# Optimization experiments

Hardware: AMD Instinct MI355X
Metric: run time of the kernel (lower is better)

Reference implementation:

```python
import jax, jax.numpy as jnp
import numpy as np

NORM_EPS = 1e-12  # torch F.normalize default eps (module's self.eps is unused)


def setup_inputs() -> dict:
    key = jax.random.key(0)
    k1, k2 = jax.random.split(key)
    src_feat = jax.random.normal(k1, (4, 2048, 128), dtype=jnp.float32)
    tgt_feat = jax.random.normal(k2, (4, 2048, 128), dtype=jnp.float32)
    return {"src_feat": src_feat, "tgt_feat": tgt_feat}


def reference(src_feat, tgt_feat):
    # src_feat: [B,N,C], tgt_feat: [B,M,C]
    # Cosine similarity via normalized matmul instead of [B,N,M,C] broadcast.
    src_sq = jnp.sum(src_feat * src_feat, axis=-1)          # [B,N]
    tgt_sq = jnp.sum(tgt_feat * tgt_feat, axis=-1)          # [B,M]
    src_n = src_feat / jnp.maximum(jnp.sqrt(src_sq), NORM_EPS)[..., None]
    tgt_n = tgt_feat / jnp.maximum(jnp.sqrt(tgt_sq), NORM_EPS)[..., None]
    cosine_sim = jnp.einsum('bnc,bmc->bnm', src_n, tgt_n)   # [B,N,M]
    # Squared L2 distance via ||s||^2 + ||t||^2 - 2 s.t (clamped for numerics)
    dots = jnp.einsum('bnc,bmc->bnm', src_feat, tgt_feat)   # [B,N,M]
    dist_sq = src_sq[:, :, None] + tgt_sq[:, None, :] - 2.0 * dots
    feat_dist = jnp.sqrt(jnp.maximum(dist_sq, 0.0))
    feat_dist_normalized = 1.0 / (1.0 + feat_dist)
    # [B,N,M,2]
    return jnp.stack([cosine_sim, feat_dist_normalized], axis=-1)
```

## Files before the change

### kernel.cpp

```cpp
#include <hip/hip_runtime.h>

#define BATCH 4
#define NDIM 2048
#define MDIM 2048
#define CDIM 128

typedef short bf16x8 __attribute__((ext_vector_type(8)));
typedef float f32x4  __attribute__((ext_vector_type(4)));

__device__ __forceinline__ unsigned short f2bf(float f) {
    union { float f; unsigned int u; } v; v.f = f;
    unsigned int u = v.u;
    return (unsigned short)((u + 0x7FFFu + ((u >> 16) & 1u)) >> 16);
}

__global__ __launch_bounds__(256) void norm_kernel(
    const float* __restrict__ src, const float* __restrict__ tgt,
    float* __restrict__ ws)
{
    int gid  = blockIdx.x * 256 + threadIdx.x;
    int wid  = gid >> 6;
    int lane = gid & 63;
    const float* base = (wid < BATCH * NDIM)
        ? (src + (size_t)wid * CDIM)
        : (tgt + (size_t)(wid - BATCH * NDIM) * CDIM);
    float2 v = ((const float2*)base)[lane];
    float s = v.x * v.x + v.y * v.y;
    #pragma unroll
    for (int off = 32; off >= 1; off >>= 1) s += __shfl_xor(s, off, 64);
    if (lane == 0) ws[wid] = s;
}

__global__ __launch_bounds__(256) void sim_mfma(
    const float* __restrict__ src, const float* __restrict__ tgt,
    const float* __restrict__ ws, float* __restrict__ out)
{
    __shared__ unsigned short As[128 * 128];
    __shared__ unsigned short Bs[128 * 128];

    const int tid = threadIdx.x;
    const int b   = blockIdx.z;
    const int i0  = blockIdx.y << 7;
    const int j0  = blockIdx.x << 7;

    const float4* s4 = (const float4*)(src + ((size_t)b * NDIM + i0) * CDIM);
    const float4* t4 = (const float4*)(tgt + ((size_t)b * MDIM + j0) * CDIM);

    #pragma unroll 4
    for (int it = 0; it < 16; ++it) {
        int idx  = tid + it * 256;
        int row  = idx >> 5;
        int c4   = idx & 31;
        float4 va = s4[idx];
        float4 vb = t4[idx];
        int chunk = c4 >> 1;
        int half  = c4 & 1;
        int off   = row * 128 + (((chunk ^ (row & 15)) << 3) + (half << 2));
        ushort4 ua, ub;
        ua.x = f2bf(va.x); ua.y = f2bf(va.y); ua.z = f2bf(va.z); ua.w = f2bf(va.w);
        ub.x = f2bf(vb.x); ub.y = f2bf(vb.y); ub.z = f2bf(vb.z); ub.w = f2bf(vb.w);
        *(ushort4*)&As[off] = ua;
        *(ushort4*)&Bs[off] = ub;
    }
    __syncthreads();

    const int wave = tid >> 6;
    const int lane = tid & 63;
    const int wm   = (wave & 1) << 6;
    const int wn   = (wave >> 1) << 6;
    const int l16  = lane & 15;
    const int q    = lane >> 4;

    f32x4 acc[4][4];
    #pragma unroll
    for (int i = 0; i < 4; ++i)
        #pragma unroll
        for (int j = 0; j < 4; ++j) acc[i][j] = (f32x4){0.f, 0.f, 0.f, 0.f};

    #pragma unroll
    for (int k0 = 0; k0 < 4; ++k0) {
        int chunk = (k0 << 2) + q;
        int swz   = (chunk ^ l16) << 3;
        bf16x8 a[4], bv[4];
        #pragma unroll
        for (int i = 0; i < 4; ++i)
            a[i] = *(const bf16x8*)&As[(wm + (i << 4) + l16) * 128 + swz];
        #pragma unroll
        for (int j = 0; j < 4; ++j)
            bv[j] = *(const bf16x8*)&Bs[(wn + (j << 4) + l16) * 128 + swz];
        #pragma unroll
        for (int i = 0; i < 4; ++i)
            #pragma unroll
            for (int j = 0; j < 4; ++j)
                acc[i][j] = __builtin_amdgcn_mfma_f32_16x16x32_bf16(
                    a[i], bv[j], acc[i][j], 0, 0, 0);
    }

    const float* nrmS = ws + (size_t)b * NDIM + i0;
    const float* nrmT = ws + (size_t)BATCH * NDIM + (size_t)b * MDIM + j0;

    float sq[4][4], isq[4][4];
    #pragma unroll
    for (int i = 0; i < 4; ++i) {
        float4 s4v = *(const float4*)&nrmS[wm + (i << 4) + (q << 2)];
        sq[i][0] = s4v.x; sq[i][1] = s4v.y; sq[i][2] = s4v.z; sq[i][3] = s4v.w;
        #pragma unroll
        for (int r = 0; r < 4; ++r)
            isq[i][r] = __builtin_amdgcn_rsqf(fmaxf(sq[i][r], 1e-24f));
    }
    float tq[4], itq[4];
    #pragma unroll
    for (int j = 0; j < 4; ++j) {
        tq[j]  = nrmT[wn + (j << 4) + l16];
        itq[j] = __builtin_amdgcn_rsqf(fmaxf(tq[j], 1e-24f));
    }

    float2* out2 = (float2*)out;
    #pragma unroll
    for (int i = 0; i < 4; ++i) {
        #pragma unroll
        for (int r = 0; r < 4; ++r) {
            int mrow = wm + (i << 4) + (q << 2) + r;
            size_t rowbase = ((size_t)b * NDIM + (size_t)(i0 + mrow)) * MDIM + j0;
            float sqr = sq[i][r], isr = isq[i][r];
            #pragma unroll
            for (int j = 0; j < 4; ++j) {
                int ncol = wn + (j << 4) + l16;
                float d   = acc[i][j][r];
                float cs  = d * isr * itq[j];
                float dsq = sqr + tq[j] - 2.0f * d;
                float fd  = __builtin_amdgcn_sqrtf(fmaxf(dsq, 0.0f));
                float fdn = __builtin_amdgcn_rcpf(1.0f + fd);
                out2[rowbase + ncol] = make_float2(cs, fdn);
            }
        }
    }
}

extern "C" void kernel_launch(void* const* d_in, const int* in_sizes, int n_in,
                              void* d_out, int out_size, void* d_ws, size_t ws_size,
                              hipStream_t stream) {
    const float* src = (const float*)d_in[0];
    const float* tgt = (const float*)d_in[1];
    float* ws  = (float*)d_ws;
    float* out = (float*)d_out;

    norm_kernel<<<dim3(4096), dim3(256), 0, stream>>>(src, tgt, ws);

    dim3 grid(MDIM / 128, NDIM / 128, BATCH);
    sim_mfma<<<grid, dim3(256), 0, stream>>>(src, tgt, ws, out);
}
```

Baseline: 147.8 us.

## Halve N tile, interleave MFMA with epilogue, widen norm kernel loads

The similarity kernel's tile shrinks from 128x128 to 128x64 and shared memory for B is halved. The launch bound now requests 3 blocks per SM, and the MFMA accumulation is split into two 16-column passes, each followed straight away by its epilogue. This cuts live accumulator registers and LDS use to raise occupancy and overlap output stores with compute, at the cost of twice as many blocks that each reload the A tile. The norm kernel now processes two rows per wave with float4 loads.

```diff
diff --git a/kernel.cpp b/kernel.cpp
--- a/kernel.cpp
+++ b/kernel.cpp
@@ -21,27 +21,28 @@
     int gid  = blockIdx.x * 256 + threadIdx.x;
     int wid  = gid >> 6;
     int lane = gid & 63;
-    const float* base = (wid < BATCH * NDIM)
-        ? (src + (size_t)wid * CDIM)
-        : (tgt + (size_t)(wid - BATCH * NDIM) * CDIM);
-    float2 v = ((const float2*)base)[lane];
-    float s = v.x * v.x + v.y * v.y;
+    int row  = (wid << 1) + (lane >> 5);
+    const float* base = (row < BATCH * NDIM)
+        ? (src + (size_t)row * CDIM)
+        : (tgt + (size_t)(row - BATCH * NDIM) * CDIM);
+    float4 v = ((const float4*)base)[lane & 31];
+    float s = v.x * v.x + v.y * v.y + v.z * v.z + v.w * v.w;
     #pragma unroll
-    for (int off = 32; off >= 1; off >>= 1) s += __shfl_xor(s, off, 64);
-    if (lane == 0) ws[wid] = s;
+    for (int off = 16; off >= 1; off >>= 1) s += __shfl_xor(s, off, 64);
+    if ((lane & 31) == 0) ws[row] = s;
 }
 
-__global__ __launch_bounds__(256) void sim_mfma(
+__global__ __launch_bounds__(256, 3) void sim_mfma(
     const float* __restrict__ src, const float* __restrict__ tgt,
     const float* __restrict__ ws, float* __restrict__ out)
 {
     __shared__ unsigned short As[128 * 128];
-    __shared__ unsigned short Bs[128 * 128];
+    __shared__ unsigned short Bs[64 * 128];
 
     const int tid = threadIdx.x;
     const int b   = blockIdx.z;
     const int i0  = blockIdx.y << 7;
-    const int j0  = blockIdx.x << 7;
+    const int j0  = blockIdx.x << 6;
 
     const float4* s4 = (const float4*)(src + ((size_t)b * NDIM + i0) * CDIM);
     const float4* t4 = (const float4*)(tgt + ((size_t)b * MDIM + j0) * CDIM);
@@ -52,14 +53,24 @@
         int row  = idx >> 5;
         int c4   = idx & 31;
         float4 va = s4[idx];
+        int chunk = c4 >> 1;
+        int half  = c4 & 1;
+        int off   = row * 128 + (((chunk ^ (row & 15)) << 3) + (half << 2));
+        ushort4 ua;
+        ua.x = f2bf(va.x); ua.y = f2bf(va.y); ua.z = f2bf(va.z); ua.w = f2bf(va.w);
+        *(ushort4*)&As[off] = ua;
+    }
+    #pragma unroll 4
+    for (int it = 0; it < 8; ++it) {
+        int idx  = tid + it * 256;
+        int row  = idx >> 5;
+        int c4   = idx & 31;
         float4 vb = t4[idx];
         int chunk = c4 >> 1;
         int half  = c4 & 1;
         int off   = row * 128 + (((chunk ^ (row & 15)) << 3) + (half << 2));
-        ushort4 ua, ub;
-        ua.x = f2bf(va.x); ua.y = f2bf(va.y); ua.z = f2bf(va.z); ua.w = f2bf(va.w);
+        ushort4 ub;
         ub.x = f2bf(vb.x); ub.y = f2bf(vb.y); ub.z = f2bf(vb.z); ub.w = f2bf(vb.w);
-        *(ushort4*)&As[off] = ua;
         *(ushort4*)&Bs[off] = ub;
     }
     __syncthreads();
@@ -67,34 +78,9 @@
     const int wave = tid >> 6;
     const int lane = tid & 63;
     const int wm   = (wave & 1) << 6;
-    const int wn   = (wave >> 1) << 6;
+    const int wn   = (wave >> 1) << 5;
     const int l16  = lane & 15;
     const int q    = lane >> 4;
-
-    f32x4 acc[4][4];
-    #pragma unroll
-    for (int i = 0; i < 4; ++i)
-        #pragma unroll
-        for (int j = 0; j < 4; ++j) acc[i][j] = (f32x4){0.f, 0.f, 0.f, 0.f};
-
-    #pragma unroll
-    for (int k0 = 0; k0 < 4; ++k0) {
-        int chunk = (k0 << 2) + q;
-        int swz   = (chunk ^ l16) << 3;
-        bf16x8 a[4], bv[4];
-        #pragma unroll
-        for (int i = 0; i < 4; ++i)
-            a[i] = *(const bf16x8*)&As[(wm + (i << 4) + l16) * 128 + swz];
-        #pragma unroll
-        for (int j = 0; j < 4; ++j)
-            bv[j] = *(const bf16x8*)&Bs[(wn + (j << 4) + l16) * 128 + swz];
-        #pragma unroll
-        for (int i = 0; i < 4; ++i)
-            #pragma unroll
-            for (int j = 0; j < 4; ++j)
-                acc[i][j] = __builtin_amdgcn_mfma_f32_16x16x32_bf16(
-                    a[i], bv[j], acc[i][j], 0, 0, 0);
-    }
 
     const float* nrmS = ws + (size_t)b * NDIM + i0;
     const float* nrmT = ws + (size_t)BATCH * NDIM + (size_t)b * MDIM + j0;
@@ -108,27 +94,46 @@
         for (int r = 0; r < 4; ++r)
             isq[i][r] = __builtin_amdgcn_rsqf(fmaxf(sq[i][r], 1e-24f));
     }
-    float tq[4], itq[4];
+    float tq[2], itq[2];
     #pragma unroll
-    for (int j = 0; j < 4; ++j) {
-        tq[j]  = nrmT[wn + (j << 4) + l16];
-        itq[j] = __builtin_amdgcn_rsqf(fmaxf(tq[j], 1e-24f));
+    for (int jh = 0; jh < 2; ++jh) {
+        tq[jh]  = nrmT[wn + (jh << 4) + l16];
+        itq[jh] = __builtin_amdgcn_rsqf(fmaxf(tq[jh], 1e-24f));
     }
 
     float2* out2 = (float2*)out;
+
     #pragma unroll
-    for (int i = 0; i < 4; ++i) {
+    for (int jh = 0; jh < 2; ++jh) {
+        f32x4 acc[4];
         #pragma unroll
-        for (int r = 0; r < 4; ++r) {
-            int mrow = wm + (i << 4) + (q << 2) + r;
-            size_t rowbase = ((size_t)b * NDIM + (size_t)(i0 + mrow)) * MDIM + j0;
-            float sqr = sq[i][r], isr = isq[i][r];
+        for (int i = 0; i < 4; ++i) acc[i] = (f32x4){0.f, 0.f, 0.f, 0.f};
+
+        const int brow = wn + (jh << 4) + l16;
+        #pragma unroll
+        for (int k0 = 0; k0 < 4; ++k0) {
+            int chunk = (k0 << 2) + q;
+            int swz   = (chunk ^ l16) << 3;
+            bf16x8 bv = *(const bf16x8*)&Bs[brow * 128 + swz];
             #pragma unroll
-            for (int j = 0; j < 4; ++j) {
-                int ncol = wn + (j << 4) + l16;
-                float d   = acc[i][j][r];
-                float cs  = d * isr * itq[j];
-                float dsq = sqr + tq[j] - 2.0f * d;
+            for (int i = 0; i < 4; ++i) {
+                bf16x8 a = *(const bf16x8*)&As[(wm + (i << 4) + l16) * 128 + swz];
+                acc[i] = __builtin_amdgcn_mfma_f32_16x16x32_bf16(a, bv, acc[i], 0, 0, 0);
+            }
+        }
+
+        const int   ncol = wn + (jh << 4) + l16;
+        const float tqj  = tq[jh], itj = itq[jh];
+        #pragma unroll
+        for (int i = 0; i < 4; ++i) {
+            #pragma unroll
+            for (int r = 0; r < 4; ++r) {
+                int mrow = wm + (i << 4) + (q << 2) + r;
+                size_t rowbase =
+                    ((size_t)b * NDIM + (size_t)(i0 + mrow)) * MDIM + j0;
+                float d   = acc[i][r];
+                float cs  = d * isq[i][r] * itj;
+                float dsq = fmaf(-2.0f, d, sq[i][r] + tqj);
                 float fd  = __builtin_amdgcn_sqrtf(fmaxf(dsq, 0.0f));
                 float fdn = __builtin_amdgcn_rcpf(1.0f + fd);
                 out2[rowbase + ncol] = make_float2(cs, fdn);
@@ -145,8 +150,8 @@
     float* ws  = (float*)d_ws;
     float* out = (float*)d_out;
 
-    norm_kernel<<<dim3(4096), dim3(256), 0, stream>>>(src, tgt, ws);
+    norm_kernel<<<dim3(2048), dim3(256), 0, stream>>>(src, tgt, ws);
 
-    dim3 grid(MDIM / 128, NDIM / 128, BATCH);
+    dim3 grid(MDIM / 64, NDIM / 128, BATCH);
     sim_mfma<<<grid, dim3(256), 0, stream>>>(src, tgt, ws, out);
 }
```

Result: no change. 147.7 us (-0.1%).
